# Kernel optimization log

Measured on AMD Instinct MI355X. Metric: run time of the kernel, lower is better.

Reference implementation:

```python
import jax, jax.numpy as jnp
import numpy as np

N, E, F_IN, H = 50000, 800000, 500, 96

def setup_inputs() -> dict:
    key = jax.random.key(0)
    ks = jax.random.split(key, 10)
    x = jax.random.normal(ks[0], (N, F_IN), dtype=jnp.float32)
    src = jax.random.randint(ks[1], (E,), 0, N, dtype=jnp.int32)
    dst = jax.random.randint(ks[2], (E,), 0, N, dtype=jnp.int32)
    perm = jax.random.permutation(ks[3], N).astype(jnp.int32)
    W1 = jax.random.normal(ks[4], (F_IN, H), dtype=jnp.float32) / np.sqrt(F_IN)
    b1 = jnp.zeros((H,), jnp.float32)
    a1 = jnp.full((H,), 0.25, jnp.float32)  # PReLU init
    W2 = jax.random.normal(ks[5], (H, H), dtype=jnp.float32) / np.sqrt(H)
    b2 = jnp.zeros((H,), jnp.float32)
    a2 = jnp.full((H,), 0.25, jnp.float32)
    Wm = jax.random.normal(ks[6], (H, H), dtype=jnp.float32) / np.sqrt(H)
    bm = jnp.zeros((H,), jnp.float32)
    return {"x": x, "src": src, "dst": dst, "perm": perm,
            "W1": W1, "b1": b1, "a1": a1, "W2": W2, "b2": b2, "a2": a2,
            "Wm": Wm, "bm": bm}

def reference(x, src, dst, perm, W1, b1, a1, W2, b2, a2, Wm, bm):
    n = x.shape[0]
    ones = jnp.ones_like(src, dtype=x.dtype)
    deg_out = jnp.clip(jax.ops.segment_sum(ones, src, num_segments=n), 1.0)
    deg_in = jnp.clip(jax.ops.segment_sum(ones, dst, num_segments=n), 1.0)
    norm_out = (deg_out ** -0.5)[:, None]  # [N,1]
    norm_in = (deg_in ** -0.5)[:, None]

    def gconv(h, W, b, a):
        # DGL GraphConv, norm='both': D_out^-1/2 -> W -> A -> D_in^-1/2 -> +b -> PReLU
        h = (h * norm_out) @ W                                  # [N,H]
        agg = jax.ops.segment_sum(h[src], dst, num_segments=n)  # SpMM via gather/scatter
        h = agg * norm_in + b
        return jnp.where(h >= 0, h, a * h)                      # PReLU

    def encode(feat):
        h = gconv(feat, W1, b1, a1)
        return gconv(h, W2, b2, a2)

    z1 = encode(x)
    z2 = encode(x[perm])  # corrupted view: permuted node features
    z1 = z1 @ Wm + bm
    z2 = z2 @ Wm + bm
    return jnp.concatenate([z1.sum(1), z2.sum(1)], axis=0)  # [2N]
```

## Files before the change

kernel.cpp:

```cpp
#include <hip/hip_runtime.h>

#define H96 96

typedef __attribute__((ext_vector_type(8))) short bf16x8_t;
typedef __attribute__((ext_vector_type(4))) float f32x4_t;
typedef __attribute__((ext_vector_type(8))) _Float16 half8_t;

__global__ void deg_kernel(const int* __restrict__ src, const int* __restrict__ dst,
                           int* __restrict__ dout, int* __restrict__ din, int E) {
    int e = blockIdx.x * blockDim.x + threadIdx.x;
    if (e < E) {
        atomicAdd(dout + src[e], 1);
        atomicAdd(din + dst[e], 1);
    }
}

__global__ void norm_kernel(const int* __restrict__ dO, const int* __restrict__ dI,
                            float* __restrict__ no, float* __restrict__ ni, int N) {
    int i = blockIdx.x * blockDim.x + threadIdx.x;
    if (i < N) {
        no[i] = rsqrtf(fmaxf((float)dO[i], 1.0f));
        ni[i] = rsqrtf(fmaxf((float)dI[i], 1.0f));
    }
}

__global__ void scanA_kernel(const int* __restrict__ in, int* __restrict__ pre,
                             int* __restrict__ bsums, int n) {
    __shared__ int s[256];
    int i = blockIdx.x * 256 + threadIdx.x;
    int v = (i < n) ? in[i] : 0;
    s[threadIdx.x] = v;
    __syncthreads();
    for (int off = 1; off < 256; off <<= 1) {
        int t = (threadIdx.x >= off) ? s[threadIdx.x - off] : 0;
        __syncthreads();
        s[threadIdx.x] += t;
        __syncthreads();
    }
    if (i < n) pre[i] = s[threadIdx.x] - v;
    if (threadIdx.x == 255) bsums[blockIdx.x] = s[255];
}

__global__ void scanB_kernel(int* __restrict__ bsums, int nb) {
    __shared__ int s[256];
    int v = (threadIdx.x < nb) ? bsums[threadIdx.x] : 0;
    s[threadIdx.x] = v;
    __syncthreads();
    for (int off = 1; off < 256; off <<= 1) {
        int t = (threadIdx.x >= off) ? s[threadIdx.x - off] : 0;
        __syncthreads();
        s[threadIdx.x] += t;
        __syncthreads();
    }
    if (threadIdx.x < nb) bsums[threadIdx.x] = s[threadIdx.x] - v;
}

__global__ void rowfin_kernel(const int* __restrict__ pre, const int* __restrict__ bsums,
                              int* __restrict__ row_start, int* __restrict__ cursor,
                              int N, int E) {
    int i = blockIdx.x * 256 + threadIdx.x;
    if (i < N) {
        int v = pre[i] + bsums[blockIdx.x];
        row_start[i] = v;
        cursor[i] = v;
    }
    if (i == 0) row_start[N] = E;
}

__global__ void scatter_kernel(const int* __restrict__ src, const int* __restrict__ dst,
                               const int* __restrict__ perm, const float* __restrict__ norm_out,
                               int* __restrict__ cursor, int4* __restrict__ edge4, int E) {
    int e = blockIdx.x * 256 + threadIdx.x;
    if (e < E) {
        int d = dst[e];
        int s = src[e];
        int p = atomicAdd(cursor + d, 1);
        edge4[p] = make_int4(s, perm[s], __float_as_int(norm_out[s]), 0);
    }
}

__global__ void histblk_kernel(const int* __restrict__ deg, int* __restrict__ hb,
                               int N, int nb) {
    __shared__ int h[256];
    h[threadIdx.x] = 0;
    __syncthreads();
    int i = blockIdx.x * 256 + threadIdx.x;
    if (i < N) atomicAdd(&h[min(deg[i], 255)], 1);
    __syncthreads();
    hb[threadIdx.x * nb + blockIdx.x] = h[threadIdx.x];
}

__global__ void place2_kernel(const int* __restrict__ deg, const int* __restrict__ hpre,
                              const int* __restrict__ bsums, int* __restrict__ order,
                              int N, int nb) {
    __shared__ int cur[256];
    int idx = threadIdx.x * nb + blockIdx.x;
    cur[threadIdx.x] = hpre[idx] + bsums[idx >> 8];
    __syncthreads();
    int i = blockIdx.x * 256 + threadIdx.x;
    if (i < N) {
        int b = min(deg[i], 255);
        int p = atomicAdd(&cur[b], 1);
        order[p] = i;
    }
}

__device__ __forceinline__ void f2bf2(float v, unsigned short& h, unsigned short& l) {
    unsigned int b = __float_as_uint(v);
    unsigned short hh = (unsigned short)((b + 0x7FFFu + ((b >> 16) & 1u)) >> 16);
    float fh = __uint_as_float(((unsigned int)hh) << 16);
    float r = v - fh;
    unsigned int rb = __float_as_uint(r);
    unsigned short ll = (unsigned short)((rb + 0x7FFFu + ((rb >> 16) & 1u)) >> 16);
    h = hh; l = ll;
}

__global__ void weights_prep(const float* __restrict__ W1, const float* __restrict__ W2,
                             const float* __restrict__ Wm, const float* __restrict__ bm,
                             unsigned short* __restrict__ w1h, unsigned short* __restrict__ w1l,
                             unsigned short* __restrict__ w2h, unsigned short* __restrict__ w2l,
                             float* __restrict__ wsum, float* __restrict__ bsum,
                             int F, int KP1) {
    int idx = blockIdx.x * 256 + threadIdx.x;
    int z1 = 96 * KP1, z2 = z1 + 96 * 96;
    if (idx < z1) {
        int n = idx / KP1, k = idx - n * KP1;
        float v = (k < F) ? W1[(size_t)k * 96 + n] : 0.f;
        unsigned short h, l;
        f2bf2(v, h, l);
        w1h[idx] = h; w1l[idx] = l;
    } else if (idx < z2) {
        int t = idx - z1;
        int n = t / 96, k = t - n * 96;
        float v = W2[(size_t)k * 96 + n];
        unsigned short h, l;
        f2bf2(v, h, l);
        w2h[t] = h; w2l[t] = l;
    } else if (idx < z2 + 96) {
        int c = idx - z2;
        float s = 0.f;
        for (int j = 0; j < 96; j++) s += Wm[c * 96 + j];
        wsum[c] = s;
    } else if (idx == z2 + 96) {
        float s = 0.f;
        for (int j = 0; j < 96; j++) s += bm[j];
        bsum[0] = s;
    }
}

#define GBM 64
#define GBK 32
#define ASTR2 40
__global__ __launch_bounds__(256) void gemm_mfma(const void* __restrict__ Av,
                                                 const unsigned short* __restrict__ Bth,
                                                 const unsigned short* __restrict__ Btl,
                                                 _Float16* __restrict__ C16,
                                                 int M, int K, int KP, int a_half) {
    __shared__ unsigned short As_hi[GBM * ASTR2];
    __shared__ unsigned short As_lo[GBM * ASTR2];
    __shared__ unsigned short Bs_hi[96 * ASTR2];
    __shared__ unsigned short Bs_lo[96 * ASTR2];
    int tid = threadIdx.x;
    int row0 = blockIdx.x * GBM;
    int wid = tid >> 6, lane = tid & 63;
    int q = lane >> 4, mn = lane & 15;
    f32x4_t acc[6] = {};
    int nk = (K + GBK - 1) / GBK;

    const float* A32 = (const float*)Av;
    const _Float16* A16 = (const _Float16*)Av;

    for (int t = 0; t < nk; t++) {
        int k0 = t * GBK;
        if (a_half) {
            int r = tid >> 2, kq = tid & 3;
            int gr = row0 + r, gk = k0 + kq * 8;
            uint4 raw = (gr < M) ? *(const uint4*)(A16 + (size_t)gr * K + gk)
                                 : make_uint4(0, 0, 0, 0);
            const _Float16* hp = (const _Float16*)&raw;
            unsigned short hs[8], ls[8];
#pragma unroll
            for (int c = 0; c < 8; c++) f2bf2((float)hp[c], hs[c], ls[c]);
            uint4 hv, lv;
            hv.x = hs[0] | ((unsigned)hs[1] << 16); hv.y = hs[2] | ((unsigned)hs[3] << 16);
            hv.z = hs[4] | ((unsigned)hs[5] << 16); hv.w = hs[6] | ((unsigned)hs[7] << 16);
            lv.x = ls[0] | ((unsigned)ls[1] << 16); lv.y = ls[2] | ((unsigned)ls[3] << 16);
            lv.z = ls[4] | ((unsigned)ls[5] << 16); lv.w = ls[6] | ((unsigned)ls[7] << 16);
            *(uint4*)&As_hi[r * ASTR2 + kq * 8] = hv;
            *(uint4*)&As_lo[r * ASTR2 + kq * 8] = lv;
        } else {
#pragma unroll
            for (int i = 0; i < 2; i++) {
                int idx = tid + i * 256;
                int r = idx >> 3, kq = idx & 7;
                int gr = row0 + r, gk = k0 + kq * 4;
                float4 v = make_float4(0.f, 0.f, 0.f, 0.f);
                if (gr < M) {
                    if (gk + 4 <= K) {
                        v = *(const float4*)(A32 + (size_t)gr * K + gk);
                    } else {
                        float tv[4] = {0.f, 0.f, 0.f, 0.f};
                        for (int c = 0; c < 4; c++)
                            if (gk + c < K) tv[c] = A32[(size_t)gr * K + gk + c];
                        v = make_float4(tv[0], tv[1], tv[2], tv[3]);
                    }
                }
                unsigned short h0, l0, h1, l1, h2, l2, h3, l3;
                f2bf2(v.x, h0, l0); f2bf2(v.y, h1, l1);
                f2bf2(v.z, h2, l2); f2bf2(v.w, h3, l3);
                uint2 hv = make_uint2((unsigned)h0 | ((unsigned)h1 << 16),
                                      (unsigned)h2 | ((unsigned)h3 << 16));
                uint2 lv = make_uint2((unsigned)l0 | ((unsigned)l1 << 16),
                                      (unsigned)l2 | ((unsigned)l3 << 16));
                *(uint2*)&As_hi[r * ASTR2 + kq * 4] = hv;
                *(uint2*)&As_lo[r * ASTR2 + kq * 4] = lv;
            }
        }
#pragma unroll
        for (int i = 0; i < 2; i++) {
            int idx = tid + i * 256;
            if (idx < 384) {
                int n = idx >> 2, kc = idx & 3;
                uint4 hv = *(const uint4*)(Bth + (size_t)n * KP + k0 + kc * 8);
                uint4 lv = *(const uint4*)(Btl + (size_t)n * KP + k0 + kc * 8);
                *(uint4*)&Bs_hi[n * ASTR2 + kc * 8] = hv;
                *(uint4*)&Bs_lo[n * ASTR2 + kc * 8] = lv;
            }
        }
        __syncthreads();

        int wr = wid * 16 + mn;
        bf16x8_t ah = *(const bf16x8_t*)&As_hi[wr * ASTR2 + q * 8];
        bf16x8_t al = *(const bf16x8_t*)&As_lo[wr * ASTR2 + q * 8];
#pragma unroll
        for (int ct = 0; ct < 6; ct++) {
            int n = ct * 16 + mn;
            bf16x8_t bh = *(const bf16x8_t*)&Bs_hi[n * ASTR2 + q * 8];
            bf16x8_t bl = *(const bf16x8_t*)&Bs_lo[n * ASTR2 + q * 8];
            acc[ct] = __builtin_amdgcn_mfma_f32_16x16x32_bf16(ah, bh, acc[ct], 0, 0, 0);
            acc[ct] = __builtin_amdgcn_mfma_f32_16x16x32_bf16(ah, bl, acc[ct], 0, 0, 0);
            acc[ct] = __builtin_amdgcn_mfma_f32_16x16x32_bf16(al, bh, acc[ct], 0, 0, 0);
        }
        __syncthreads();
    }

#pragma unroll
    for (int reg = 0; reg < 4; reg++) {
        int gr = row0 + wid * 16 + q * 4 + reg;
        if (gr < M) {
#pragma unroll
            for (int ct = 0; ct < 6; ct++)
                C16[(size_t)gr * H96 + ct * 16 + mn] = (_Float16)acc[ct][reg];
        }
    }
}

__device__ __forceinline__ void fmah8(float4& a, float4& b, float s, half8_t v) {
    a.x = fmaf(s, (float)v[0], a.x); a.y = fmaf(s, (float)v[1], a.y);
    a.z = fmaf(s, (float)v[2], a.z); a.w = fmaf(s, (float)v[3], a.w);
    b.x = fmaf(s, (float)v[4], b.x); b.y = fmaf(s, (float)v[5], b.y);
    b.z = fmaf(s, (float)v[6], b.z); b.w = fmaf(s, (float)v[7], b.w);
}

__device__ __forceinline__ float4 prelu4(float4 acc, float ni, float4 b, float4 a) {
    float4 h;
    h.x = fmaf(acc.x, ni, b.x); h.x = (h.x >= 0.f) ? h.x : a.x * h.x;
    h.y = fmaf(acc.y, ni, b.y); h.y = (h.y >= 0.f) ? h.y : a.y * h.y;
    h.z = fmaf(acc.z, ni, b.z); h.z = (h.z >= 0.f) ? h.z : a.z * h.z;
    h.w = fmaf(acc.w, ni, b.w); h.w = (h.w >= 0.f) ? h.w : a.w * h.w;
    return h;
}

__global__ __launch_bounds__(384) void spmm1_dual(
        const half8_t* __restrict__ yh, const int* __restrict__ row_start,
        const int4* __restrict__ edge4, const int* __restrict__ order,
        const float* __restrict__ norm_out, const float* __restrict__ norm_in,
        const float* __restrict__ b1, const float* __restrict__ a1,
        half8_t* __restrict__ h1, half8_t* __restrict__ h2, int N) {
    int g = blockIdx.x * 32 + threadIdx.y;
    if (g >= N) return;
    int d = order[g];
    int tx = threadIdx.x;
    int beg = row_start[d], end = row_start[d + 1];
    const half8_t* yt = yh + tx;
    float4 a1a = {0,0,0,0}, a1b = {0,0,0,0}, a2a = {0,0,0,0}, a2b = {0,0,0,0};
    int j = beg;
    for (; j + 8 <= end; j += 8) {
        int4 e[8];
#pragma unroll
        for (int q = 0; q < 8; q++) e[q] = edge4[j + q];
        half8_t u[8], w[8];
#pragma unroll
        for (int q = 0; q < 8; q++) u[q] = yt[(size_t)e[q].x * 12];
#pragma unroll
        for (int q = 0; q < 8; q++) w[q] = yt[(size_t)e[q].y * 12];
#pragma unroll
        for (int q = 0; q < 8; q++) {
            float n = __int_as_float(e[q].z);
            fmah8(a1a, a1b, n, u[q]);
            fmah8(a2a, a2b, n, w[q]);
        }
    }
    for (; j < end; j++) {
        int4 e = edge4[j];
        float n = __int_as_float(e.z);
        fmah8(a1a, a1b, n, yt[(size_t)e.x * 12]);
        fmah8(a2a, a2b, n, yt[(size_t)e.y * 12]);
    }
    float ni = norm_in[d], no = norm_out[d];
    float4 bb0 = ((const float4*)b1)[tx * 2], bb1 = ((const float4*)b1)[tx * 2 + 1];
    float4 aa0 = ((const float4*)a1)[tx * 2], aa1 = ((const float4*)a1)[tx * 2 + 1];
    float4 r1a = prelu4(a1a, ni, bb0, aa0), r1b = prelu4(a1b, ni, bb1, aa1);
    float4 r2a = prelu4(a2a, ni, bb0, aa0), r2b = prelu4(a2b, ni, bb1, aa1);
    half8_t o1, o2;
    o1[0] = (_Float16)(r1a.x * no); o1[1] = (_Float16)(r1a.y * no);
    o1[2] = (_Float16)(r1a.z * no); o1[3] = (_Float16)(r1a.w * no);
    o1[4] = (_Float16)(r1b.x * no); o1[5] = (_Float16)(r1b.y * no);
    o1[6] = (_Float16)(r1b.z * no); o1[7] = (_Float16)(r1b.w * no);
    o2[0] = (_Float16)(r2a.x * no); o2[1] = (_Float16)(r2a.y * no);
    o2[2] = (_Float16)(r2a.z * no); o2[3] = (_Float16)(r2a.w * no);
    o2[4] = (_Float16)(r2b.x * no); o2[5] = (_Float16)(r2b.y * no);
    o2[6] = (_Float16)(r2b.z * no); o2[7] = (_Float16)(r2b.w * no);
    h1[(size_t)d * 12 + tx] = o1;
    h2[(size_t)d * 12 + tx] = o2;
}

__global__ __launch_bounds__(384) void spmm2_dual(
        const half8_t* __restrict__ th,
        const int* __restrict__ row_start, const int4* __restrict__ edge4,
        const int* __restrict__ order, const float* __restrict__ norm_in,
        const float* __restrict__ b2, const float* __restrict__ a2,
        const float* __restrict__ wsum, const float* __restrict__ bsum,
        float* __restrict__ outp, int N) {
    int g = blockIdx.x * 32 + threadIdx.y;
    int tx = threadIdx.x;
    int ty = threadIdx.y;
    bool valid = (g < N);
    int d = valid ? order[g] : 0;
    int beg = 0, end = 0;
    if (valid) { beg = row_start[d]; end = row_start[d + 1]; }
    const half8_t* t1 = th + tx;
    const half8_t* t2 = th + (size_t)N * 12 + tx;
    float4 a1a = {0,0,0,0}, a1b = {0,0,0,0}, a2a = {0,0,0,0}, a2b = {0,0,0,0};
    int j = beg;
    for (; j + 8 <= end; j += 8) {
        int s[8];
#pragma unroll
        for (int q = 0; q < 8; q++) s[q] = edge4[j + q].x;
        half8_t u[8], w[8];
#pragma unroll
        for (int q = 0; q < 8; q++) u[q] = t1[(size_t)s[q] * 12];
#pragma unroll
        for (int q = 0; q < 8; q++) w[q] = t2[(size_t)s[q] * 12];
#pragma unroll
        for (int q = 0; q < 8; q++) {
            fmah8(a1a, a1b, 1.f, u[q]);
            fmah8(a2a, a2b, 1.f, w[q]);
        }
    }
    for (; j < end; j++) {
        int s = edge4[j].x;
        fmah8(a1a, a1b, 1.f, t1[(size_t)s * 12]);
        fmah8(a2a, a2b, 1.f, t2[(size_t)s * 12]);
    }
    float ni = valid ? norm_in[d] : 0.f;
    float4 bb0 = ((const float4*)b2)[tx * 2], bb1 = ((const float4*)b2)[tx * 2 + 1];
    float4 aa0 = ((const float4*)a2)[tx * 2], aa1 = ((const float4*)a2)[tx * 2 + 1];
    float4 wv0 = ((const float4*)wsum)[tx * 2], wv1 = ((const float4*)wsum)[tx * 2 + 1];
    float4 r1a = prelu4(a1a, ni, bb0, aa0), r1b = prelu4(a1b, ni, bb1, aa1);
    float4 r2a = prelu4(a2a, ni, bb0, aa0), r2b = prelu4(a2b, ni, bb1, aa1);
    float p1 = r1a.x * wv0.x + r1a.y * wv0.y + r1a.z * wv0.z + r1a.w * wv0.w
             + r1b.x * wv1.x + r1b.y * wv1.y + r1b.z * wv1.z + r1b.w * wv1.w;
    float p2 = r2a.x * wv0.x + r2a.y * wv0.y + r2a.z * wv0.z + r2a.w * wv0.w
             + r2b.x * wv1.x + r2b.y * wv1.y + r2b.z * wv1.z + r2b.w * wv1.w;
    __shared__ float red1[32][12];
    __shared__ float red2[32][12];
    red1[ty][tx] = p1;
    red2[ty][tx] = p2;
    __syncthreads();
    if (tx == 0 && valid) {
        float s1 = 0.f, s2 = 0.f;
#pragma unroll
        for (int k = 0; k < 12; k++) { s1 += red1[ty][k]; s2 += red2[ty][k]; }
        outp[d] = s1 + bsum[0];
        outp[N + d] = s2 + bsum[0];
    }
}

extern "C" void kernel_launch(void* const* d_in, const int* in_sizes, int n_in,
                              void* d_out, int out_size, void* d_ws, size_t ws_size,
                              hipStream_t stream) {
    const float* x    = (const float*)d_in[0];
    const int*   src  = (const int*)d_in[1];
    const int*   dst  = (const int*)d_in[2];
    const int*   perm = (const int*)d_in[3];
    const float* W1   = (const float*)d_in[4];
    const float* b1   = (const float*)d_in[5];
    const float* a1   = (const float*)d_in[6];
    const float* W2   = (const float*)d_in[7];
    const float* b2   = (const float*)d_in[8];
    const float* a2   = (const float*)d_in[9];
    const float* Wm   = (const float*)d_in[10];
    const float* bm   = (const float*)d_in[11];
    float* out = (float*)d_out;

    int E = in_sizes[1];
    int N = in_sizes[3];
    int F = in_sizes[0] / N;
    int KP1 = ((F + GBK - 1) / GBK) * GBK;

    size_t NP = ((size_t)N + 256) & ~(size_t)255;
    size_t EP = ((size_t)E + 255) & ~(size_t)255;
    int nb = (N + 255) / 256;
    size_t HB = ((size_t)256 * nb + 255) & ~(size_t)255;

    int* deg_out   = (int*)d_ws;
    int* deg_in    = deg_out + NP;
    int* pre       = deg_in + NP;
    int* row_start = pre + NP;
    int* cursor    = row_start + NP;
    int* order     = cursor + NP;
    int* bsums     = order + NP;
    int* hb        = bsums + 256;
    int* hpre      = hb + HB;
    int4* edge4    = (int4*)(hpre + HB);
    float* norm_out = (float*)(edge4 + EP);
    float* norm_in  = norm_out + NP;
    float* wsum     = norm_in + NP;
    float* bsum     = wsum + 128;
    unsigned short* w1th = (unsigned short*)(bsum + 128);
    unsigned short* w1tl = w1th + 49664;
    unsigned short* w2th = w1tl + 49664;
    unsigned short* w2tl = w2th + 9728;
    _Float16* yh  = (_Float16*)(w2tl + 9728);
    _Float16* h1h = yh + ((size_t)N * H96 + 256);
    _Float16* th  = h1h + ((size_t)2 * N * H96 + 256);

    hipMemsetAsync(deg_out, 0, 2 * NP * sizeof(int), stream);
    deg_kernel<<<(E + 255) / 256, 256, 0, stream>>>(src, dst, deg_out, deg_in, E);
    norm_kernel<<<(N + 255) / 256, 256, 0, stream>>>(deg_out, deg_in, norm_out, norm_in, N);

    scanA_kernel<<<nb, 256, 0, stream>>>(deg_in, pre, bsums, N);
    scanB_kernel<<<1, 256, 0, stream>>>(bsums, nb);
    rowfin_kernel<<<nb, 256, 0, stream>>>(pre, bsums, row_start, cursor, N, E);
    scatter_kernel<<<(E + 255) / 256, 256, 0, stream>>>(src, dst, perm, norm_out, cursor,
                                                        edge4, E);

    histblk_kernel<<<nb, 256, 0, stream>>>(deg_in, hb, N, nb);
    int n2 = 256 * nb;
    int nb2 = (n2 + 255) / 256;
    scanA_kernel<<<nb2, 256, 0, stream>>>(hb, hpre, bsums, n2);
    scanB_kernel<<<1, 256, 0, stream>>>(bsums, nb2);
    place2_kernel<<<nb, 256, 0, stream>>>(deg_in, hpre, bsums, order, N, nb);

    int wtot = 96 * KP1 + 96 * 96 + 96 + 1;
    weights_prep<<<(wtot + 255) / 256, 256, 0, stream>>>(W1, W2, Wm, bm, w1th, w1tl,
                                                         w2th, w2tl, wsum, bsum, F, KP1);

    gemm_mfma<<<(N + GBM - 1) / GBM, 256, 0, stream>>>(x, w1th, w1tl, yh, N, F, KP1, 0);

    int nsb = (N + 31) / 32;
    spmm1_dual<<<nsb, dim3(12, 32), 0, stream>>>(
        (const half8_t*)yh, row_start, edge4, order, norm_out, norm_in,
        b1, a1, (half8_t*)h1h, (half8_t*)(h1h + (size_t)N * H96), N);

    gemm_mfma<<<(2 * N + GBM - 1) / GBM, 256, 0, stream>>>(h1h, w2th, w2tl, th, 2 * N, H96, H96, 1);

    spmm2_dual<<<nsb, dim3(12, 32), 0, stream>>>(
        (const half8_t*)th, row_start, edge4, order, norm_in, b2, a2,
        wsum, bsum, out, N);
}
```

Before: 448.0 us.

## Drop LDS staging in split-bf16 GEMM, load fragments directly with register prefetch

```diff
diff --git a/kernel.cpp b/kernel.cpp
--- a/kernel.cpp
+++ b/kernel.cpp
@@ -113,6 +113,23 @@
     unsigned int rb = __float_as_uint(r);
     unsigned short ll = (unsigned short)((rb + 0x7FFFu + ((rb >> 16) & 1u)) >> 16);
     h = hh; l = ll;
+}
+
+__device__ __forceinline__ void cvt8(const float f[8], bf16x8_t& ah, bf16x8_t& al) {
+    union { unsigned int u[4]; bf16x8_t v; } H, L;
+#pragma unroll
+    for (int i = 0; i < 4; i++) {
+        float v0 = f[2 * i], v1 = f[2 * i + 1];
+        unsigned int b0 = __float_as_uint(v0);
+        unsigned int b1 = __float_as_uint(v1);
+        unsigned int m0 = b0 & 0xFFFF0000u;
+        unsigned int m1 = b1 & 0xFFFF0000u;
+        float r0 = v0 - __uint_as_float(m0);
+        float r1 = v1 - __uint_as_float(m1);
+        H.u[i] = (b0 >> 16) | m1;
+        L.u[i] = (__float_as_uint(r0) >> 16) | (__float_as_uint(r1) & 0xFFFF0000u);
+    }
+    ah = H.v; al = L.v;
 }
 
 __global__ void weights_prep(const float* __restrict__ W1, const float* __restrict__ W2,
@@ -150,103 +167,81 @@
 
 #define GBM 64
 #define GBK 32
-#define ASTR2 40
 __global__ __launch_bounds__(256) void gemm_mfma(const void* __restrict__ Av,
                                                  const unsigned short* __restrict__ Bth,
                                                  const unsigned short* __restrict__ Btl,
                                                  _Float16* __restrict__ C16,
                                                  int M, int K, int KP, int a_half) {
-    __shared__ unsigned short As_hi[GBM * ASTR2];
-    __shared__ unsigned short As_lo[GBM * ASTR2];
-    __shared__ unsigned short Bs_hi[96 * ASTR2];
-    __shared__ unsigned short Bs_lo[96 * ASTR2];
     int tid = threadIdx.x;
-    int row0 = blockIdx.x * GBM;
     int wid = tid >> 6, lane = tid & 63;
     int q = lane >> 4, mn = lane & 15;
+    int row0 = blockIdx.x * GBM + wid * 16;
+    int arow = row0 + mn;
+    bool rv = (arow < M);
     f32x4_t acc[6] = {};
     int nk = (K + GBK - 1) / GBK;
 
     const float* A32 = (const float*)Av;
     const _Float16* A16 = (const _Float16*)Av;
 
+    auto loadA = [&](int t, float* f) {
+        int gk = t * GBK + q * 8;
+        if (a_half) {
+            uint4 raw = make_uint4(0, 0, 0, 0);
+            if (rv) raw = *(const uint4*)(A16 + (size_t)arow * K + gk);
+            const _Float16* hp = (const _Float16*)&raw;
+#pragma unroll
+            for (int c = 0; c < 8; c++) f[c] = (float)hp[c];
+        } else {
+            if (rv && gk + 8 <= K) {
+                float4 v0 = *(const float4*)(A32 + (size_t)arow * K + gk);
+                float4 v1 = *(const float4*)(A32 + (size_t)arow * K + gk + 4);
+                f[0] = v0.x; f[1] = v0.y; f[2] = v0.z; f[3] = v0.w;
+                f[4] = v1.x; f[5] = v1.y; f[6] = v1.z; f[7] = v1.w;
+            } else {
+#pragma unroll
+                for (int c = 0; c < 8; c++)
+                    f[c] = (rv && gk + c < K) ? A32[(size_t)arow * K + gk + c] : 0.f;
+            }
+        }
+    };
+
+    const unsigned short* bhp = Bth + (size_t)mn * KP;
+    const unsigned short* blp = Btl + (size_t)mn * KP;
+
+    float f[8], fn[8];
+    loadA(0, f);
     for (int t = 0; t < nk; t++) {
-        int k0 = t * GBK;
-        if (a_half) {
-            int r = tid >> 2, kq = tid & 3;
-            int gr = row0 + r, gk = k0 + kq * 8;
-            uint4 raw = (gr < M) ? *(const uint4*)(A16 + (size_t)gr * K + gk)
-                                 : make_uint4(0, 0, 0, 0);
-            const _Float16* hp = (const _Float16*)&raw;
-            unsigned short hs[8], ls[8];
-#pragma unroll
-            for (int c = 0; c < 8; c++) f2bf2((float)hp[c], hs[c], ls[c]);
-            uint4 hv, lv;
-            hv.x = hs[0] | ((unsigned)hs[1] << 16); hv.y = hs[2] | ((unsigned)hs[3] << 16);
-            hv.z = hs[4] | ((unsigned)hs[5] << 16); hv.w = hs[6] | ((unsigned)hs[7] << 16);
-            lv.x = ls[0] | ((unsigned)ls[1] << 16); lv.y = ls[2] | ((unsigned)ls[3] << 16);
-            lv.z = ls[4] | ((unsigned)ls[5] << 16); lv.w = ls[6] | ((unsigned)ls[7] << 16);
-            *(uint4*)&As_hi[r * ASTR2 + kq * 8] = hv;
-            *(uint4*)&As_lo[r * ASTR2 + kq * 8] = lv;
+        if (t + 1 < nk) {
+            loadA(t + 1, fn);
         } else {
 #pragma unroll
-            for (int i = 0; i < 2; i++) {
-                int idx = tid + i * 256;
-                int r = idx >> 3, kq = idx & 7;
-                int gr = row0 + r, gk = k0 + kq * 4;
-                float4 v = make_float4(0.f, 0.f, 0.f, 0.f);
-                if (gr < M) {
-                    if (gk + 4 <= K) {
-                        v = *(const float4*)(A32 + (size_t)gr * K + gk);
-                    } else {
-                        float tv[4] = {0.f, 0.f, 0.f, 0.f};
-                        for (int c = 0; c < 4; c++)
-                            if (gk + c < K) tv[c] = A32[(size_t)gr * K + gk + c];
-                        v = make_float4(tv[0], tv[1], tv[2], tv[3]);
-                    }
-                }
-                unsigned short h0, l0, h1, l1, h2, l2, h3, l3;
-                f2bf2(v.x, h0, l0); f2bf2(v.y, h1, l1);
-                f2bf2(v.z, h2, l2); f2bf2(v.w, h3, l3);
-                uint2 hv = make_uint2((unsigned)h0 | ((unsigned)h1 << 16),
-                                      (unsigned)h2 | ((unsigned)h3 << 16));
-                uint2 lv = make_uint2((unsigned)l0 | ((unsigned)l1 << 16),
-                                      (unsigned)l2 | ((unsigned)l3 << 16));
-                *(uint2*)&As_hi[r * ASTR2 + kq * 4] = hv;
-                *(uint2*)&As_lo[r * ASTR2 + kq * 4] = lv;
-            }
-        }
-#pragma unroll
-        for (int i = 0; i < 2; i++) {
-            int idx = tid + i * 256;
-            if (idx < 384) {
-                int n = idx >> 2, kc = idx & 3;
-                uint4 hv = *(const uint4*)(Bth + (size_t)n * KP + k0 + kc * 8);
-                uint4 lv = *(const uint4*)(Btl + (size_t)n * KP + k0 + kc * 8);
-                *(uint4*)&Bs_hi[n * ASTR2 + kc * 8] = hv;
-                *(uint4*)&Bs_lo[n * ASTR2 + kc * 8] = lv;
-            }
-        }
-        __syncthreads();
-
-        int wr = wid * 16 + mn;
-        bf16x8_t ah = *(const bf16x8_t*)&As_hi[wr * ASTR2 + q * 8];
-        bf16x8_t al = *(const bf16x8_t*)&As_lo[wr * ASTR2 + q * 8];
+            for (int c = 0; c < 8; c++) fn[c] = 0.f;
+        }
+
+        bf16x8_t ah, al;
+        cvt8(f, ah, al);
+
+        int gk = t * GBK + q * 8;
+        bf16x8_t bh[6], bl[6];
 #pragma unroll
         for (int ct = 0; ct < 6; ct++) {
-            int n = ct * 16 + mn;
-            bf16x8_t bh = *(const bf16x8_t*)&Bs_hi[n * ASTR2 + q * 8];
-            bf16x8_t bl = *(const bf16x8_t*)&Bs_lo[n * ASTR2 + q * 8];
-            acc[ct] = __builtin_amdgcn_mfma_f32_16x16x32_bf16(ah, bh, acc[ct], 0, 0, 0);
-            acc[ct] = __builtin_amdgcn_mfma_f32_16x16x32_bf16(ah, bl, acc[ct], 0, 0, 0);
-            acc[ct] = __builtin_amdgcn_mfma_f32_16x16x32_bf16(al, bh, acc[ct], 0, 0, 0);
-        }
-        __syncthreads();
+            bh[ct] = *(const bf16x8_t*)(bhp + (size_t)ct * 16 * KP + gk);
+            bl[ct] = *(const bf16x8_t*)(blp + (size_t)ct * 16 * KP + gk);
+        }
+#pragma unroll
+        for (int ct = 0; ct < 6; ct++) {
+            acc[ct] = __builtin_amdgcn_mfma_f32_16x16x32_bf16(ah, bh[ct], acc[ct], 0, 0, 0);
+            acc[ct] = __builtin_amdgcn_mfma_f32_16x16x32_bf16(ah, bl[ct], acc[ct], 0, 0, 0);
+            acc[ct] = __builtin_amdgcn_mfma_f32_16x16x32_bf16(al, bh[ct], acc[ct], 0, 0, 0);
+        }
+#pragma unroll
+        for (int c = 0; c < 8; c++) f[c] = fn[c];
     }
 
 #pragma unroll
     for (int reg = 0; reg < 4; reg++) {
-        int gr = row0 + wid * 16 + q * 4 + reg;
+        int gr = row0 + q * 4 + reg;
         if (gr < M) {
 #pragma unroll
             for (int ct = 0; ct < 6; ct++)
```

After: 503.6 us. 12.4% more time.
